# Kernel optimization log

Measured on AMD Instinct MI355X. Metric: run time of the kernel, lower is better.

The kernel has to match this reference:

```python
import jax, jax.numpy as jnp
import numpy as np

N_NODES = 100000


def gcn_conv(x, src, dst, deg_inv_sqrt, W, b):
    # x: [N, Fin], src/dst: [E_total] (self-loops included), W: [Fin, Fout]
    h = x @ W                                  # [N, Fout]
    norm = deg_inv_sqrt[src] * deg_inv_sqrt[dst]  # [E_total]
    msgs = h[src] * norm[:, None]              # [E_total, Fout] gather
    out = jax.ops.segment_sum(msgs, dst, num_segments=N_NODES)  # scatter-add
    return out + b


def setup_inputs() -> dict:
    key = jax.random.key(0)
    k1, k2, k3, k4, k5, k6, k7, k8 = jax.random.split(key, 8)
    input_dim, hidden_dim, out_dim = 4, 64, 2
    n_edges = 3200000
    x = jax.random.normal(k1, (N_NODES, input_dim), dtype=jnp.float32)
    edge_index = jax.random.randint(k2, (2, n_edges), 0, N_NODES, dtype=jnp.int64)
    s1 = 1.0 / np.sqrt(input_dim)
    s2 = 1.0 / np.sqrt(hidden_dim)
    W1 = jax.random.uniform(k3, (input_dim, hidden_dim), jnp.float32, -s1, s1)
    b1 = jnp.zeros((hidden_dim,), jnp.float32)
    W2 = jax.random.uniform(k4, (hidden_dim, hidden_dim), jnp.float32, -s2, s2)
    b2 = jnp.zeros((hidden_dim,), jnp.float32)
    Wf = jax.random.uniform(k5, (hidden_dim, out_dim), jnp.float32, -s2, s2)
    bf = jax.random.uniform(k6, (out_dim,), jnp.float32, -s2, s2)
    return {"x": x, "edge_index": edge_index, "W1": W1, "b1": b1,
            "W2": W2, "b2": b2, "Wf": Wf, "bf": bf}


def reference(x, edge_index, W1, b1, W2, b2, Wf, bf):
    # Add self-loops (PyG GCNConv default)
    loop = jnp.arange(N_NODES, dtype=edge_index.dtype)
    src = jnp.concatenate([edge_index[0], loop])
    dst = jnp.concatenate([edge_index[1], loop])
    # Symmetric normalization: degree on destination after self-loops
    deg = jax.ops.segment_sum(jnp.ones_like(dst, dtype=x.dtype), dst,
                              num_segments=N_NODES)
    deg_inv_sqrt = jnp.where(deg > 0, jax.lax.rsqrt(deg), 0.0)
    h = jax.nn.relu(gcn_conv(x, src, dst, deg_inv_sqrt, W1, b1))
    h = jax.nn.relu(gcn_conv(h, src, dst, deg_inv_sqrt, W2, b2))
    return h @ Wf + bf
```

## Files before the change

### kernel.cpp

```cpp
#include <hip/hip_runtime.h>
#include <hip/hip_bf16.h>

#define N_NODES 100000
#define N_EDGES 3200000
#define NB ((N_NODES + 255) / 256)
#define NBUCKET NB
#define EPB 8192
#define NPB ((N_EDGES + EPB - 1) / EPB)
#define BCAP 11264

__device__ inline unsigned f2bf(float f) {
  unsigned x = __float_as_uint(f);
  return (x + 0x7FFFu + ((x >> 16) & 1u)) >> 16;
}


__global__ void __launch_bounds__(256) k_pass1(const int* __restrict__ src,
                                               const int* __restrict__ dst,
                                               int* __restrict__ gcur,
                                               unsigned int* __restrict__ eb) {
  __shared__ int hist[NBUCKET];
  __shared__ int gbase[NBUCKET];
  int tid = threadIdx.x;
  int base = blockIdx.x * EPB;
  int cnt = min(EPB, N_EDGES - base);
  int n4 = cnt >> 2;
  for (int i = tid; i < NBUCKET; i += 256) hist[i] = 0;
  __syncthreads();
  const int4* d4 = (const int4*)(dst + base);
  const int4* s4 = (const int4*)(src + base);
  unsigned mv[32];
  unsigned short mb[32];
#pragma unroll
  for (int k = 0; k < 8; ++k) {
    int i = tid + (k << 8);
    if (i < n4) {
      int4 dv = d4[i];
      int4 sv = s4[i];
      int b0 = dv.x >> 8, b1_ = dv.y >> 8, b2 = dv.z >> 8, b3 = dv.w >> 8;
      unsigned p0 = atomicAdd(&hist[b0], 1);
      unsigned p1 = atomicAdd(&hist[b1_], 1);
      unsigned p2 = atomicAdd(&hist[b2], 1);
      unsigned p3 = atomicAdd(&hist[b3], 1);
      mv[4 * k + 0] = (unsigned)sv.x | ((unsigned)(dv.x & 255) << 17) | (p0 << 25);
      mv[4 * k + 1] = (unsigned)sv.y | ((unsigned)(dv.y & 255) << 17) | (p1 << 25);
      mv[4 * k + 2] = (unsigned)sv.z | ((unsigned)(dv.z & 255) << 17) | (p2 << 25);
      mv[4 * k + 3] = (unsigned)sv.w | ((unsigned)(dv.w & 255) << 17) | (p3 << 25);
      mb[4 * k + 0] = (unsigned short)b0;
      mb[4 * k + 1] = (unsigned short)b1_;
      mb[4 * k + 2] = (unsigned short)b2;
      mb[4 * k + 3] = (unsigned short)b3;
    } else {
      mb[4 * k + 0] = 0xFFFF; mb[4 * k + 1] = 0xFFFF;
      mb[4 * k + 2] = 0xFFFF; mb[4 * k + 3] = 0xFFFF;
    }
  }
  __syncthreads();
  for (int b = tid; b < NBUCKET; b += 256) {
    int h = hist[b];
    gbase[b] = h ? atomicAdd(&gcur[b], h) : 0;
  }
  __syncthreads();
#pragma unroll
  for (int k = 0; k < 32; ++k) {
    if (mb[k] != 0xFFFF) {
      int b = mb[k];
      unsigned v = mv[k];
      unsigned pos = (unsigned)gbase[b] + (v >> 25);
      if (pos < BCAP) eb[(size_t)b * BCAP + pos] = v & 0x01FFFFFFu;
    }
  }
}


__global__ void __launch_bounds__(256) k_part2(unsigned int* __restrict__ eb,
                                               const int* __restrict__ gcur,
                                               int* __restrict__ rs, int* __restrict__ re,
                                               float* __restrict__ dis,
                                               const float4* __restrict__ x4,
                                               float4* __restrict__ xd) {
  __shared__ int hist[256], scn[256], cur[256];
  __shared__ int tot;
  __shared__ unsigned int stage[BCAP];
  int b = blockIdx.x, tid = threadIdx.x;
  int n0 = b << 8;
  int cnt = gcur[b];
  int base = b * BCAP;
  hist[tid] = 0; cur[tid] = 0;
  __syncthreads();
  for (int i = tid; i < cnt; i += 256)
    atomicAdd(&hist[eb[base + i] >> 17], 1);
  __syncthreads();
  int n = n0 + tid;
  int deg = hist[tid];
  int slots = (n < N_NODES) ? ((deg + 1 + 7) & ~7) : 0;
  int x = slots;
  scn[tid] = x;
  __syncthreads();
  for (int off = 1; off < 256; off <<= 1) {
    int t = (tid >= off) ? scn[tid - off] : 0;
    __syncthreads();
    x += t; scn[tid] = x;
    __syncthreads();
  }
  int excl = x - slots;
  if (tid == 255) tot = x;
  if (n < N_NODES) {
    rs[n]  = base + excl;
    re[n]  = base + excl + deg + 1;
    float dn = rsqrtf((float)(deg + 1));
    dis[n] = dn;
    float4 xv = x4[n];
    float4 w; w.x = xv.x * dn; w.y = xv.y * dn; w.z = xv.z * dn; w.w = xv.w * dn;
    xd[n] = w;
    stage[excl] = (unsigned)n;
    for (int i = deg + 1; i < slots; ++i)
      stage[excl + i] = (unsigned)N_NODES;
  }
  if (b == 0 && tid == 0) xd[N_NODES] = make_float4(0.f, 0.f, 0.f, 0.f);
  scn[tid] = excl + 1;
  __syncthreads();
  for (int i = tid; i < cnt; i += 256) {
    unsigned v = eb[base + i];
    unsigned low = v >> 17;
    int lpos = scn[low] + atomicAdd(&cur[low], 1);
    stage[lpos] = v & 0x1FFFFu;
  }
  __syncthreads();
  int total = tot;
  for (int i = tid; i < total; i += 256)
    eb[base + i] = stage[i];
  if (tid < 16) {
    int gp = total + tid;
    if (gp < BCAP) eb[base + gp] = (unsigned)N_NODES;
  }
}


__global__ void __launch_bounds__(256) k_l1(const float4* __restrict__ xd,
                                            const float* __restrict__ dis,
                                            const int* __restrict__ rs,
                                            const int* __restrict__ re,
                                            const int* __restrict__ csr,
                                            const float* __restrict__ W1,
                                            const float* __restrict__ b1,
                                            unsigned int* __restrict__ h1o) {
  int gt = blockIdx.x * 256 + threadIdx.x;
  int nid = gt >> 2, p = gt & 3;
  if (nid > N_NODES) return;
  if (nid == N_NODES) {
    uint4 z = make_uint4(0u, 0u, 0u, 0u);
    uint4* op = (uint4*)(h1o + nid * 32 + p * 8);
    op[0] = z; op[1] = z;
    return;
  }
  int e0 = rs[nid];
  int it4 = ((re[nid] - e0 + 7) & ~7) >> 2;
  const int* cp = csr + e0 + p;
  float ax = 0.f, ay = 0.f, az = 0.f, aw = 0.f;
#pragma unroll 4
  for (int t = 0; t < it4; ++t) {
    int s = cp[t << 2];
    float4 v = xd[s];
    ax += v.x; ay += v.y; az += v.z; aw += v.w;
  }
  ax += __shfl_xor(ax, 1); ax += __shfl_xor(ax, 2);
  ay += __shfl_xor(ay, 1); ay += __shfl_xor(ay, 2);
  az += __shfl_xor(az, 1); az += __shfl_xor(az, 2);
  aw += __shfl_xor(aw, 1); aw += __shfl_xor(aw, 2);
  float dn = dis[nid];
  ax *= dn; ay *= dn; az *= dn; aw *= dn;
  int j0 = p << 4;
  unsigned ou[8];
#pragma unroll
  for (int j2 = 0; j2 < 8; ++j2) {
    int j = j0 + j2 * 2;
    float s0 = b1[j]     + ax * W1[j]     + ay * W1[64 + j]     + az * W1[128 + j]     + aw * W1[192 + j];
    float s1 = b1[j + 1] + ax * W1[j + 1] + ay * W1[64 + j + 1] + az * W1[128 + j + 1] + aw * W1[192 + j + 1];
    unsigned u0 = f2bf(fmaxf(s0, 0.f) * dn);
    unsigned u1 = f2bf(fmaxf(s1, 0.f) * dn);
    ou[j2] = u0 | (u1 << 16);
  }
  uint4* op = (uint4*)(h1o + nid * 32 + p * 8);
  op[0] = make_uint4(ou[0], ou[1], ou[2], ou[3]);
  op[1] = make_uint4(ou[4], ou[5], ou[6], ou[7]);
}


__device__ inline void acc_bf2(float& a0, float& a1, unsigned u) {
  a0 += __uint_as_float(u << 16);
  a1 += __uint_as_float(u & 0xffff0000u);
}

__global__ void __launch_bounds__(256)
k_layer2(const __hip_bfloat16* __restrict__ h1s, const float* __restrict__ dis,
         const int* __restrict__ rs, const int* __restrict__ re,
         const int* __restrict__ csr,
         const float* __restrict__ W2, const float* __restrict__ b2,
         const float* __restrict__ Wf, const float* __restrict__ bf,
         float* __restrict__ out) {
  __shared__ float sh[4][64];
  int l = threadIdx.x & 63;
  int w = threadIdx.x >> 6;
  int n = blockIdx.x * 4 + w;
  int g = l >> 3;
  int c = l & 7;

  const unsigned int* h32 = (const unsigned int*)h1s;
  int e0 = rs[n];
  int iter = (re[n] - e0 + 7) >> 3;
  const int* cb = csr + e0 + g;
  int coff = c << 2;

  float a0 = 0.f, a1 = 0.f, a2 = 0.f, a3 = 0.f;
  float a4 = 0.f, a5 = 0.f, a6 = 0.f, a7 = 0.f;
  int sc = cb[0];
  int sn = cb[8];
  uint4 u = *(const uint4*)(h32 + (sc << 5) + coff);
  for (int it = 1; it < iter; ++it) {
    int sf = cb[(it + 1) << 3];
    uint4 r = *(const uint4*)(h32 + (sn << 5) + coff);
    acc_bf2(a0, a1, u.x); acc_bf2(a2, a3, u.y);
    acc_bf2(a4, a5, u.z); acc_bf2(a6, a7, u.w);
    u = r; sn = sf;
  }
  acc_bf2(a0, a1, u.x); acc_bf2(a2, a3, u.y);
  acc_bf2(a4, a5, u.z); acc_bf2(a6, a7, u.w);

#define RED3(a) a += __shfl_xor(a, 8); a += __shfl_xor(a, 16); a += __shfl_xor(a, 32);
  RED3(a0) RED3(a1) RED3(a2) RED3(a3) RED3(a4) RED3(a5) RED3(a6) RED3(a7)
#undef RED3

  float dn = dis[n];
  if (l < 8) {
    float4 v0; v0.x = a0 * dn; v0.y = a1 * dn; v0.z = a2 * dn; v0.w = a3 * dn;
    float4 v1; v1.x = a4 * dn; v1.y = a5 * dn; v1.z = a6 * dn; v1.w = a7 * dn;
    *(float4*)&sh[w][(l << 3) + 0] = v0;
    *(float4*)&sh[w][(l << 3) + 4] = v1;
  }
  __syncthreads();

  float t = b2[l];
  const float4* shv = (const float4*)sh[w];
#pragma unroll 4
  for (int j4 = 0; j4 < 16; ++j4) {
    float4 a4v = shv[j4];
    t += a4v.x * W2[(4 * j4 + 0) * 64 + l];
    t += a4v.y * W2[(4 * j4 + 1) * 64 + l];
    t += a4v.z * W2[(4 * j4 + 2) * 64 + l];
    t += a4v.w * W2[(4 * j4 + 3) * 64 + l];
  }
  t = fmaxf(t, 0.0f);

  float p0 = t * Wf[l * 2 + 0];
  float p1 = t * Wf[l * 2 + 1];
  for (int off = 32; off; off >>= 1) {
    p0 += __shfl_down(p0, off);
    p1 += __shfl_down(p1, off);
  }
  if (l == 0) {
    out[n * 2 + 0] = p0 + bf[0];
    out[n * 2 + 1] = p1 + bf[1];
  }
}


extern "C" void kernel_launch(void* const* d_in, const int* in_sizes, int n_in,
                              void* d_out, int out_size, void* d_ws, size_t ws_size,
                              hipStream_t stream) {
  const float* x  = (const float*)d_in[0];
  const int*   ei = (const int*)d_in[1];
  const float* W1 = (const float*)d_in[2];
  const float* b1 = (const float*)d_in[3];
  const float* W2 = (const float*)d_in[4];
  const float* b2 = (const float*)d_in[5];
  const float* Wf = (const float*)d_in[6];
  const float* bf = (const float*)d_in[7];
  float* out = (float*)d_out;

  const int* srcv = ei;
  const int* dstv = ei + N_EDGES;

  char* p = (char*)d_ws;
  auto take = [&](size_t bytes) { char* r = p; p += (bytes + 255) & ~(size_t)255; return r; };
  int*          gcur = (int*)take((size_t)NBUCKET * 4);
  unsigned int* eb   = (unsigned int*)take((size_t)NBUCKET * BCAP * 4 + 512);
  int*          rs   = (int*)take((size_t)N_NODES * 4);
  int*          re   = (int*)take((size_t)N_NODES * 4);
  float*        dis  = (float*)take((size_t)N_NODES * 4);
  float4*       xd   = (float4*)take((size_t)(N_NODES + 1) * 16);
  __hip_bfloat16* h1s = (__hip_bfloat16*)take((size_t)(N_NODES + 1) * 64 * 2);

  (void)hipMemsetAsync(gcur, 0, (size_t)NBUCKET * 4, stream);
  k_pass1<<<NPB, 256, 0, stream>>>(srcv, dstv, gcur, eb);
  k_part2<<<NBUCKET, 256, 0, stream>>>(eb, gcur, rs, re, dis, (const float4*)x, xd);
  const int* csr = (const int*)eb;
  k_l1<<<((N_NODES + 1) * 4 + 255) / 256, 256, 0, stream>>>(xd, dis, rs, re, csr, W1, b1, (unsigned int*)h1s);
  k_layer2<<<N_NODES / 4, 256, 0, stream>>>(h1s, dis, rs, re, csr, W2, b2, Wf, bf, out);
}
```

Before: 246.6 us.

## Fuse layer-1 aggregation into CSR build using global degree atomics

Per-node degrees are now counted with global atomics during the bucketing pass. That removes the histogram pre-pass over each bucket in k_part2, and a small k_prep kernel computes the normalisation and the scaled features. The layer-1 gather, transform and bf16 store move into k_part2, which reads neighbour indices straight from the shared-memory stage buffer, so the k_l1 kernel and its CSR re-read go away. In exchange it adds 3.2M global atomics, an extra launch, and one thread per node in the layer-1 gather instead of four, which may hurt load balance and latency hiding.

Result: slower. 347.3 us (+40.8%).

```diff
diff --git a/kernel.cpp b/kernel.cpp
--- a/kernel.cpp
+++ b/kernel.cpp
@@ -3,8 +3,7 @@
 
 #define N_NODES 100000
 #define N_EDGES 3200000
-#define NB ((N_NODES + 255) / 256)
-#define NBUCKET NB
+#define NBUCKET 391
 #define EPB 8192
 #define NPB ((N_EDGES + EPB - 1) / EPB)
 #define BCAP 11264
@@ -18,6 +17,7 @@
 __global__ void __launch_bounds__(256) k_pass1(const int* __restrict__ src,
                                                const int* __restrict__ dst,
                                                int* __restrict__ gcur,
+                                               int* __restrict__ deg,
                                                unsigned int* __restrict__ eb) {
   __shared__ int hist[NBUCKET];
   __shared__ int gbase[NBUCKET];
@@ -38,6 +38,10 @@
       int4 dv = d4[i];
       int4 sv = s4[i];
       int b0 = dv.x >> 8, b1_ = dv.y >> 8, b2 = dv.z >> 8, b3 = dv.w >> 8;
+      atomicAdd(&deg[dv.x], 1);
+      atomicAdd(&deg[dv.y], 1);
+      atomicAdd(&deg[dv.z], 1);
+      atomicAdd(&deg[dv.w], 1);
       unsigned p0 = atomicAdd(&hist[b0], 1);
       unsigned p1 = atomicAdd(&hist[b1_], 1);
       unsigned p2 = atomicAdd(&hist[b2], 1);
@@ -73,26 +77,45 @@
 }
 
 
+__global__ void __launch_bounds__(256) k_prep(const int* __restrict__ deg,
+                                              const float4* __restrict__ x4,
+                                              float* __restrict__ dis,
+                                              float4* __restrict__ xd,
+                                              unsigned int* __restrict__ h1o) {
+  int nid = blockIdx.x * 256 + threadIdx.x;
+  if (nid < N_NODES) {
+    float dn = rsqrtf((float)(deg[nid] + 1));
+    dis[nid] = dn;
+    float4 xv = x4[nid];
+    float4 w; w.x = xv.x * dn; w.y = xv.y * dn; w.z = xv.z * dn; w.w = xv.w * dn;
+    xd[nid] = w;
+  } else if (nid == N_NODES) {
+    xd[N_NODES] = make_float4(0.f, 0.f, 0.f, 0.f);
+    uint4 z = make_uint4(0u, 0u, 0u, 0u);
+    uint4* op = (uint4*)(h1o + (size_t)N_NODES * 32);
+#pragma unroll
+    for (int i = 0; i < 8; ++i) op[i] = z;
+  }
+}
+
+
 __global__ void __launch_bounds__(256) k_part2(unsigned int* __restrict__ eb,
                                                const int* __restrict__ gcur,
+                                               const int* __restrict__ deg_g,
                                                int* __restrict__ rs, int* __restrict__ re,
-                                               float* __restrict__ dis,
-                                               const float4* __restrict__ x4,
-                                               float4* __restrict__ xd) {
-  __shared__ int hist[256], scn[256], cur[256];
+                                               const float4* __restrict__ xd,
+                                               const float* __restrict__ W1,
+                                               const float* __restrict__ b1,
+                                               unsigned int* __restrict__ h1o) {
+  __shared__ int scn[256], cur[256];
   __shared__ int tot;
   __shared__ unsigned int stage[BCAP];
   int b = blockIdx.x, tid = threadIdx.x;
   int n0 = b << 8;
-  int cnt = gcur[b];
+  int cnt = min(gcur[b], BCAP);
   int base = b * BCAP;
-  hist[tid] = 0; cur[tid] = 0;
-  __syncthreads();
-  for (int i = tid; i < cnt; i += 256)
-    atomicAdd(&hist[eb[base + i] >> 17], 1);
-  __syncthreads();
   int n = n0 + tid;
-  int deg = hist[tid];
+  int deg = (n < N_NODES) ? deg_g[n] : 0;
   int slots = (n < N_NODES) ? ((deg + 1 + 7) & ~7) : 0;
   int x = slots;
   scn[tid] = x;
@@ -106,24 +129,18 @@
   int excl = x - slots;
   if (tid == 255) tot = x;
   if (n < N_NODES) {
-    rs[n]  = base + excl;
-    re[n]  = base + excl + deg + 1;
-    float dn = rsqrtf((float)(deg + 1));
-    dis[n] = dn;
-    float4 xv = x4[n];
-    float4 w; w.x = xv.x * dn; w.y = xv.y * dn; w.z = xv.z * dn; w.w = xv.w * dn;
-    xd[n] = w;
+    rs[n] = base + excl;
+    re[n] = base + excl + deg + 1;
     stage[excl] = (unsigned)n;
     for (int i = deg + 1; i < slots; ++i)
       stage[excl + i] = (unsigned)N_NODES;
   }
-  if (b == 0 && tid == 0) xd[N_NODES] = make_float4(0.f, 0.f, 0.f, 0.f);
-  scn[tid] = excl + 1;
+  cur[tid] = excl + 1;
   __syncthreads();
   for (int i = tid; i < cnt; i += 256) {
     unsigned v = eb[base + i];
     unsigned low = v >> 17;
-    int lpos = scn[low] + atomicAdd(&cur[low], 1);
+    int lpos = atomicAdd(&cur[low], 1);
     stage[lpos] = v & 0x1FFFFu;
   }
   __syncthreads();
@@ -134,56 +151,38 @@
     int gp = total + tid;
     if (gp < BCAP) eb[base + gp] = (unsigned)N_NODES;
   }
-}
-
-
-__global__ void __launch_bounds__(256) k_l1(const float4* __restrict__ xd,
-                                            const float* __restrict__ dis,
-                                            const int* __restrict__ rs,
-                                            const int* __restrict__ re,
-                                            const int* __restrict__ csr,
-                                            const float* __restrict__ W1,
-                                            const float* __restrict__ b1,
-                                            unsigned int* __restrict__ h1o) {
-  int gt = blockIdx.x * 256 + threadIdx.x;
-  int nid = gt >> 2, p = gt & 3;
-  if (nid > N_NODES) return;
-  if (nid == N_NODES) {
-    uint4 z = make_uint4(0u, 0u, 0u, 0u);
-    uint4* op = (uint4*)(h1o + nid * 32 + p * 8);
-    op[0] = z; op[1] = z;
-    return;
-  }
-  int e0 = rs[nid];
-  int it4 = ((re[nid] - e0 + 7) & ~7) >> 2;
-  const int* cp = csr + e0 + p;
-  float ax = 0.f, ay = 0.f, az = 0.f, aw = 0.f;
-#pragma unroll 4
-  for (int t = 0; t < it4; ++t) {
-    int s = cp[t << 2];
-    float4 v = xd[s];
-    ax += v.x; ay += v.y; az += v.z; aw += v.w;
-  }
-  ax += __shfl_xor(ax, 1); ax += __shfl_xor(ax, 2);
-  ay += __shfl_xor(ay, 1); ay += __shfl_xor(ay, 2);
-  az += __shfl_xor(az, 1); az += __shfl_xor(az, 2);
-  aw += __shfl_xor(aw, 1); aw += __shfl_xor(aw, 2);
-  float dn = dis[nid];
-  ax *= dn; ay *= dn; az *= dn; aw *= dn;
-  int j0 = p << 4;
-  unsigned ou[8];
-#pragma unroll
-  for (int j2 = 0; j2 < 8; ++j2) {
-    int j = j0 + j2 * 2;
-    float s0 = b1[j]     + ax * W1[j]     + ay * W1[64 + j]     + az * W1[128 + j]     + aw * W1[192 + j];
-    float s1 = b1[j + 1] + ax * W1[j + 1] + ay * W1[64 + j + 1] + az * W1[128 + j + 1] + aw * W1[192 + j + 1];
-    unsigned u0 = f2bf(fmaxf(s0, 0.f) * dn);
-    unsigned u1 = f2bf(fmaxf(s1, 0.f) * dn);
-    ou[j2] = u0 | (u1 << 16);
-  }
-  uint4* op = (uint4*)(h1o + nid * 32 + p * 8);
-  op[0] = make_uint4(ou[0], ou[1], ou[2], ou[3]);
-  op[1] = make_uint4(ou[4], ou[5], ou[6], ou[7]);
+
+  if (n < N_NODES) {
+    float ax = 0.f, ay = 0.f, az = 0.f, aw = 0.f;
+    int e8 = slots >> 3;
+    for (int t = 0; t < e8; ++t) {
+      int p0 = excl + (t << 3);
+#pragma unroll
+      for (int q = 0; q < 8; ++q) {
+        unsigned s = stage[p0 + q];
+        float4 v = xd[s];
+        ax += v.x; ay += v.y; az += v.z; aw += v.w;
+      }
+    }
+    float dn = rsqrtf((float)(deg + 1));
+    ax *= dn; ay *= dn; az *= dn; aw *= dn;
+    uint4* op = (uint4*)(h1o + (size_t)n * 32);
+#pragma unroll
+    for (int grp = 0; grp < 4; ++grp) {
+      unsigned ou[8];
+#pragma unroll
+      for (int j2 = 0; j2 < 8; ++j2) {
+        int j = grp * 16 + j2 * 2;
+        float s0 = b1[j]     + ax * W1[j]     + ay * W1[64 + j]     + az * W1[128 + j]     + aw * W1[192 + j];
+        float s1 = b1[j + 1] + ax * W1[j + 1] + ay * W1[64 + j + 1] + az * W1[128 + j + 1] + aw * W1[192 + j + 1];
+        unsigned u0 = f2bf(fmaxf(s0, 0.f) * dn);
+        unsigned u1 = f2bf(fmaxf(s1, 0.f) * dn);
+        ou[j2] = u0 | (u1 << 16);
+      }
+      op[grp * 2 + 0] = make_uint4(ou[0], ou[1], ou[2], ou[3]);
+      op[grp * 2 + 1] = make_uint4(ou[4], ou[5], ou[6], ou[7]);
+    }
+  }
 }
 
 
@@ -284,6 +283,7 @@
   char* p = (char*)d_ws;
   auto take = [&](size_t bytes) { char* r = p; p += (bytes + 255) & ~(size_t)255; return r; };
   int*          gcur = (int*)take((size_t)NBUCKET * 4);
+  int*          deg  = (int*)take((size_t)N_NODES * 4);
   unsigned int* eb   = (unsigned int*)take((size_t)NBUCKET * BCAP * 4 + 512);
   int*          rs   = (int*)take((size_t)N_NODES * 4);
   int*          re   = (int*)take((size_t)N_NODES * 4);
@@ -291,10 +291,11 @@
   float4*       xd   = (float4*)take((size_t)(N_NODES + 1) * 16);
   __hip_bfloat16* h1s = (__hip_bfloat16*)take((size_t)(N_NODES + 1) * 64 * 2);
 
-  (void)hipMemsetAsync(gcur, 0, (size_t)NBUCKET * 4, stream);
-  k_pass1<<<NPB, 256, 0, stream>>>(srcv, dstv, gcur, eb);
-  k_part2<<<NBUCKET, 256, 0, stream>>>(eb, gcur, rs, re, dis, (const float4*)x, xd);
+  size_t zlen = (size_t)((char*)deg - (char*)gcur) + (size_t)N_NODES * 4;
+  (void)hipMemsetAsync(gcur, 0, zlen, stream);
+  k_pass1<<<NPB, 256, 0, stream>>>(srcv, dstv, gcur, deg, eb);
+  k_prep <<<(N_NODES + 256) / 256, 256, 0, stream>>>(deg, (const float4*)x, dis, xd, (unsigned int*)h1s);
+  k_part2<<<NBUCKET, 256, 0, stream>>>(eb, gcur, deg, rs, re, (const float4*)xd, W1, b1, (unsigned int*)h1s);
   const int* csr = (const int*)eb;
-  k_l1<<<((N_NODES + 1) * 4 + 255) / 256, 256, 0, stream>>>(xd, dis, rs, re, csr, W1, b1, (unsigned int*)h1s);
   k_layer2<<<N_NODES / 4, 256, 0, stream>>>(h1s, dis, rs, re, csr, W2, b2, Wf, bf, out);
 }
```

## Recompute layer-1 hidden features per edge from 4-dim aggregates instead of storing 64-dim bf16

Applied to the files above, without the earlier changes.

Layer 1 now stores only the normalized 4-dimensional aggregate and the node's deg_inv_sqrt (32 bytes per node) rather than the 64-wide bf16 hidden vector (128 bytes). Layer 2 gathers this compact record per edge and recomputes W1 projection, bias, ReLU and scaling inline, with each lane owning one output feature. This cuts gather bandwidth and removes the bf16 rounding, but every lane re-reads the same two float4 per edge and does extra FMAs per edge. The edge loop is now serial per wavefront, two edges at a time, instead of spreading eight edges across lane groups. Bucket count is hard-coded and the per-bucket count is clamped to capacity.

After: 366.0 us. 48.4% more time.

```diff
diff --git a/kernel.cpp b/kernel.cpp
--- a/kernel.cpp
+++ b/kernel.cpp
@@ -1,18 +1,11 @@
 #include <hip/hip_runtime.h>
-#include <hip/hip_bf16.h>
 
 #define N_NODES 100000
 #define N_EDGES 3200000
-#define NB ((N_NODES + 255) / 256)
-#define NBUCKET NB
+#define NBUCKET 391
 #define EPB 8192
 #define NPB ((N_EDGES + EPB - 1) / EPB)
 #define BCAP 11264
-
-__device__ inline unsigned f2bf(float f) {
-  unsigned x = __float_as_uint(f);
-  return (x + 0x7FFFu + ((x >> 16) & 1u)) >> 16;
-}
 
 
 __global__ void __launch_bounds__(256) k_pass1(const int* __restrict__ src,
@@ -84,7 +77,7 @@
   __shared__ unsigned int stage[BCAP];
   int b = blockIdx.x, tid = threadIdx.x;
   int n0 = b << 8;
-  int cnt = gcur[b];
+  int cnt = min(gcur[b], BCAP);
   int base = b * BCAP;
   hist[tid] = 0; cur[tid] = 0;
   __syncthreads();
@@ -142,16 +135,12 @@
                                             const int* __restrict__ rs,
                                             const int* __restrict__ re,
                                             const int* __restrict__ csr,
-                                            const float* __restrict__ W1,
-                                            const float* __restrict__ b1,
-                                            unsigned int* __restrict__ h1o) {
+                                            float4* __restrict__ qd) {
   int gt = blockIdx.x * 256 + threadIdx.x;
   int nid = gt >> 2, p = gt & 3;
   if (nid > N_NODES) return;
   if (nid == N_NODES) {
-    uint4 z = make_uint4(0u, 0u, 0u, 0u);
-    uint4* op = (uint4*)(h1o + nid * 32 + p * 8);
-    op[0] = z; op[1] = z;
+    if (p < 2) qd[(size_t)nid * 2 + p] = make_float4(0.f, 0.f, 0.f, 0.f);
     return;
   }
   int e0 = rs[nid];
@@ -169,33 +158,16 @@
   az += __shfl_xor(az, 1); az += __shfl_xor(az, 2);
   aw += __shfl_xor(aw, 1); aw += __shfl_xor(aw, 2);
   float dn = dis[nid];
-  ax *= dn; ay *= dn; az *= dn; aw *= dn;
-  int j0 = p << 4;
-  unsigned ou[8];
-#pragma unroll
-  for (int j2 = 0; j2 < 8; ++j2) {
-    int j = j0 + j2 * 2;
-    float s0 = b1[j]     + ax * W1[j]     + ay * W1[64 + j]     + az * W1[128 + j]     + aw * W1[192 + j];
-    float s1 = b1[j + 1] + ax * W1[j + 1] + ay * W1[64 + j + 1] + az * W1[128 + j + 1] + aw * W1[192 + j + 1];
-    unsigned u0 = f2bf(fmaxf(s0, 0.f) * dn);
-    unsigned u1 = f2bf(fmaxf(s1, 0.f) * dn);
-    ou[j2] = u0 | (u1 << 16);
-  }
-  uint4* op = (uint4*)(h1o + nid * 32 + p * 8);
-  op[0] = make_uint4(ou[0], ou[1], ou[2], ou[3]);
-  op[1] = make_uint4(ou[4], ou[5], ou[6], ou[7]);
-}
-
-
-__device__ inline void acc_bf2(float& a0, float& a1, unsigned u) {
-  a0 += __uint_as_float(u << 16);
-  a1 += __uint_as_float(u & 0xffff0000u);
-}
+  if (p == 0) qd[(size_t)nid * 2]     = make_float4(ax * dn, ay * dn, az * dn, aw * dn);
+  if (p == 1) qd[(size_t)nid * 2 + 1] = make_float4(dn, 0.f, 0.f, 0.f);
+}
+
 
 __global__ void __launch_bounds__(256)
-k_layer2(const __hip_bfloat16* __restrict__ h1s, const float* __restrict__ dis,
+k_layer2(const float4* __restrict__ qd, const float* __restrict__ dis,
          const int* __restrict__ rs, const int* __restrict__ re,
          const int* __restrict__ csr,
+         const float* __restrict__ W1, const float* __restrict__ b1,
          const float* __restrict__ W2, const float* __restrict__ b2,
          const float* __restrict__ Wf, const float* __restrict__ bf,
          float* __restrict__ out) {
@@ -203,41 +175,31 @@
   int l = threadIdx.x & 63;
   int w = threadIdx.x >> 6;
   int n = blockIdx.x * 4 + w;
-  int g = l >> 3;
-  int c = l & 7;
-
-  const unsigned int* h32 = (const unsigned int*)h1s;
-  int e0 = rs[n];
-  int iter = (re[n] - e0 + 7) >> 3;
-  const int* cb = csr + e0 + g;
-  int coff = c << 2;
-
-  float a0 = 0.f, a1 = 0.f, a2 = 0.f, a3 = 0.f;
-  float a4 = 0.f, a5 = 0.f, a6 = 0.f, a7 = 0.f;
-  int sc = cb[0];
-  int sn = cb[8];
-  uint4 u = *(const uint4*)(h32 + (sc << 5) + coff);
-  for (int it = 1; it < iter; ++it) {
-    int sf = cb[(it + 1) << 3];
-    uint4 r = *(const uint4*)(h32 + (sn << 5) + coff);
-    acc_bf2(a0, a1, u.x); acc_bf2(a2, a3, u.y);
-    acc_bf2(a4, a5, u.z); acc_bf2(a6, a7, u.w);
-    u = r; sn = sf;
-  }
-  acc_bf2(a0, a1, u.x); acc_bf2(a2, a3, u.y);
-  acc_bf2(a4, a5, u.z); acc_bf2(a6, a7, u.w);
-
-#define RED3(a) a += __shfl_xor(a, 8); a += __shfl_xor(a, 16); a += __shfl_xor(a, 32);
-  RED3(a0) RED3(a1) RED3(a2) RED3(a3) RED3(a4) RED3(a5) RED3(a6) RED3(a7)
-#undef RED3
-
-  float dn = dis[n];
-  if (l < 8) {
-    float4 v0; v0.x = a0 * dn; v0.y = a1 * dn; v0.z = a2 * dn; v0.w = a3 * dn;
-    float4 v1; v1.x = a4 * dn; v1.y = a5 * dn; v1.z = a6 * dn; v1.w = a7 * dn;
-    *(float4*)&sh[w][(l << 3) + 0] = v0;
-    *(float4*)&sh[w][(l << 3) + 4] = v1;
-  }
+
+  float w0 = W1[l], w1 = W1[64 + l], w2 = W1[128 + l], w3 = W1[192 + l];
+  float bj = b1[l];
+
+  int e = rs[n], e1 = re[n];
+  float acc0 = 0.f, acc1 = 0.f;
+  for (; e + 1 < e1; e += 2) {
+    int s0 = csr[e], s1 = csr[e + 1];
+    float4 q0 = qd[(size_t)s0 * 2];
+    float4 d0 = qd[(size_t)s0 * 2 + 1];
+    float4 q1 = qd[(size_t)s1 * 2];
+    float4 d1 = qd[(size_t)s1 * 2 + 1];
+    float h0 = bj + q0.x * w0 + q0.y * w1 + q0.z * w2 + q0.w * w3;
+    float h1 = bj + q1.x * w0 + q1.y * w1 + q1.z * w2 + q1.w * w3;
+    acc0 += fmaxf(h0 * d0.x, 0.f);
+    acc1 += fmaxf(h1 * d1.x, 0.f);
+  }
+  if (e < e1) {
+    int s = csr[e];
+    float4 q = qd[(size_t)s * 2];
+    float4 d = qd[(size_t)s * 2 + 1];
+    float h = bj + q.x * w0 + q.y * w1 + q.z * w2 + q.w * w3;
+    acc0 += fmaxf(h * d.x, 0.f);
+  }
+  sh[w][l] = (acc0 + acc1) * dis[n];
   __syncthreads();
 
   float t = b2[l];
@@ -289,12 +251,12 @@
   int*          re   = (int*)take((size_t)N_NODES * 4);
   float*        dis  = (float*)take((size_t)N_NODES * 4);
   float4*       xd   = (float4*)take((size_t)(N_NODES + 1) * 16);
-  __hip_bfloat16* h1s = (__hip_bfloat16*)take((size_t)(N_NODES + 1) * 64 * 2);
+  float4*       qd   = (float4*)take((size_t)(N_NODES + 1) * 32);
 
   (void)hipMemsetAsync(gcur, 0, (size_t)NBUCKET * 4, stream);
   k_pass1<<<NPB, 256, 0, stream>>>(srcv, dstv, gcur, eb);
   k_part2<<<NBUCKET, 256, 0, stream>>>(eb, gcur, rs, re, dis, (const float4*)x, xd);
   const int* csr = (const int*)eb;
-  k_l1<<<((N_NODES + 1) * 4 + 255) / 256, 256, 0, stream>>>(xd, dis, rs, re, csr, W1, b1, (unsigned int*)h1s);
-  k_layer2<<<N_NODES / 4, 256, 0, stream>>>(h1s, dis, rs, re, csr, W2, b2, Wf, bf, out);
-}
+  k_l1<<<((N_NODES + 1) * 4 + 255) / 256, 256, 0, stream>>>(xd, dis, rs, re, csr, qd);
+  k_layer2<<<N_NODES / 4, 256, 0, stream>>>(qd, dis, rs, re, csr, W1, b1, W2, b2, Wf, bf, out);
+}
```
